# Kernel tuning notes

Hardware: AMD Instinct MI355X
Metric: run time of the kernel (lower is better)

## Reference

```python
import jax, jax.numpy as jnp
import numpy as np

EPS = 1e-5

def setup_inputs() -> dict:
    key = jax.random.key(0)
    k1, k2, k3, k4, k5 = jax.random.split(key, 5)
    x = jax.random.normal(k1, (2048, 64, 768), dtype=jnp.float32)
    ln_w = jnp.ones((768,), dtype=jnp.float32)
    ln_b = jnp.zeros((768,), dtype=jnp.float32)
    # nn.Linear default init: U(-1/sqrt(in), 1/sqrt(in))
    bound = 1.0 / np.sqrt(768.0)
    W = jax.random.uniform(k2, (64, 768), dtype=jnp.float32, minval=-bound, maxval=bound)
    b = jax.random.uniform(k3, (64,), dtype=jnp.float32, minval=-bound, maxval=bound)
    return {"x": x, "ln_w": ln_w, "ln_b": ln_b, "W": W, "b": b}

def reference(x, ln_w, ln_b, W, b):
    B = x.shape[0]
    # LayerNorm over last dim (768)
    mu = jnp.mean(x, axis=-1, keepdims=True)
    var = jnp.mean(jnp.square(x - mu), axis=-1, keepdims=True)
    xn = (x - mu) * jax.lax.rsqrt(var + EPS) * ln_w + ln_b
    # Linear 768 -> 64, then SiLU
    y = jnp.einsum('bch,oh->bco', xn, W) + b
    y = y * jax.nn.sigmoid(y)
    # unpatchify: [B,64,64] -> [B,8,8,4,4,4] -> permute(0,3,1,4,2,5) -> [B,4,32,32]
    y = y.reshape(B, 8, 8, 4, 4, 4)
    y = jnp.transpose(y, (0, 3, 1, 4, 2, 5))
    return y.reshape(B, 4, 32, 32)
```

## Files before the change

kernel.cpp:

```cpp
#include <hip/hip_runtime.h>
#include <hip/hip_bf16.h>
#include <cstdint>

typedef __attribute__((ext_vector_type(8))) short s16x8;
typedef __attribute__((ext_vector_type(4))) float f32x4;

union CV2 { __hip_bfloat162 h; uint32_t u; };

__global__ void prep_kernel(const float* __restrict__ W,
                            const float* __restrict__ lnw,
                            const float* __restrict__ lnb,
                            const float* __restrict__ bias,
                            __hip_bfloat16* __restrict__ Wb,
                            float* __restrict__ Ssum,
                            float* __restrict__ bp) {
    const int o = blockIdx.x;
    const int tid = threadIdx.x;
    float s = 0.f, bb = 0.f;
    for (int k = tid; k < 768; k += 256) {
        float wraw = W[o * 768 + k];
        float wv = lnw[k] * wraw;
        s += wv;
        bb += lnb[k] * wraw;
        int kk = k >> 5, rem = k & 31;
        int q = rem >> 3, j = rem & 7;
        int t = o >> 4, n = o & 15;
        int l = q * 16 + n;
        Wb[(kk * 4 + t) * 512 + l * 8 + j] = __float2bfloat16(wv);
    }
    __shared__ float rs[4], rb[4];
    for (int off = 32; off > 0; off >>= 1) {
        s  += __shfl_down(s, off);
        bb += __shfl_down(bb, off);
    }
    int wid = tid >> 6;
    if ((tid & 63) == 0) { rs[wid] = s; rb[wid] = bb; }
    __syncthreads();
    if (tid == 0) {
        Ssum[o] = rs[0] + rs[1] + rs[2] + rs[3];
        bp[o]   = bias[o] + rb[0] + rb[1] + rb[2] + rb[3];
    }
}

__global__ __launch_bounds__(256, 3) void fused_kernel(
        const float* __restrict__ x,
        const uint4* __restrict__ Wb4,
        const float* __restrict__ Ssum,
        const float* __restrict__ bp,
        float* __restrict__ out) {
    const int b   = blockIdx.x;
    const int tid = threadIdx.x;
    const int w   = tid >> 6;
    const int l   = tid & 63;
    const int q   = l >> 4;
    const int n   = l & 15;

    __shared__ __align__(16) float sout[4096];

    const float* xr = x + (size_t)b * 49152 + (w * 16 + n) * 768 + q * 8;
    const uint4* Wl = Wb4 + l;

    f32x4 acc0 = {0.f, 0.f, 0.f, 0.f};
    f32x4 acc1 = acc0, acc2 = acc0, acc3 = acc0;
    float sum = 0.f, ssq = 0.f;

    float4 cur[8], nxt[8];
    #pragma unroll
    for (int s = 0; s < 4; s++) {
        cur[2 * s]     = *(const float4*)(xr + s * 32);
        cur[2 * s + 1] = *(const float4*)(xr + s * 32 + 4);
    }

    #pragma unroll
    for (int c = 0; c < 6; c++) {
        s16x8 af[4];
        #pragma unroll
        for (int s = 0; s < 4; s++) {
            float4 lo = cur[2 * s], hi = cur[2 * s + 1];
            sum += lo.x; ssq = fmaf(lo.x, lo.x, ssq);
            sum += lo.y; ssq = fmaf(lo.y, lo.y, ssq);
            sum += lo.z; ssq = fmaf(lo.z, lo.z, ssq);
            sum += lo.w; ssq = fmaf(lo.w, lo.w, ssq);
            sum += hi.x; ssq = fmaf(hi.x, hi.x, ssq);
            sum += hi.y; ssq = fmaf(hi.y, hi.y, ssq);
            sum += hi.z; ssq = fmaf(hi.z, hi.z, ssq);
            sum += hi.w; ssq = fmaf(hi.w, hi.w, ssq);
            CV2 p0, p1, p2, p3;
            p0.h = __float22bfloat162_rn(make_float2(lo.x, lo.y));
            p1.h = __float22bfloat162_rn(make_float2(lo.z, lo.w));
            p2.h = __float22bfloat162_rn(make_float2(hi.x, hi.y));
            p3.h = __float22bfloat162_rn(make_float2(hi.z, hi.w));
            af[s] = __builtin_bit_cast(s16x8,
                        make_uint4(p0.u, p1.u, p2.u, p3.u));
        }

        if (c < 5) {
            #pragma unroll
            for (int s = 0; s < 4; s++) {
                nxt[2 * s]     = *(const float4*)(xr + (c + 1) * 128 + s * 32);
                nxt[2 * s + 1] = *(const float4*)(xr + (c + 1) * 128 + s * 32 + 4);
            }
        }

        #pragma unroll
        for (int s = 0; s < 4; s++) {
            uint4 wb0 = Wl[((c * 4 + s) * 4 + 0) * 64];
            uint4 wb1 = Wl[((c * 4 + s) * 4 + 1) * 64];
            uint4 wb2 = Wl[((c * 4 + s) * 4 + 2) * 64];
            uint4 wb3 = Wl[((c * 4 + s) * 4 + 3) * 64];
            acc0 = __builtin_amdgcn_mfma_f32_16x16x32_bf16(
                       af[s], __builtin_bit_cast(s16x8, wb0), acc0, 0, 0, 0);
            acc1 = __builtin_amdgcn_mfma_f32_16x16x32_bf16(
                       af[s], __builtin_bit_cast(s16x8, wb1), acc1, 0, 0, 0);
            acc2 = __builtin_amdgcn_mfma_f32_16x16x32_bf16(
                       af[s], __builtin_bit_cast(s16x8, wb2), acc2, 0, 0, 0);
            acc3 = __builtin_amdgcn_mfma_f32_16x16x32_bf16(
                       af[s], __builtin_bit_cast(s16x8, wb3), acc3, 0, 0, 0);
        }

        if (c < 5) {
            #pragma unroll
            for (int i = 0; i < 8; i++) cur[i] = nxt[i];
        }
    }

    sum += __shfl_xor(sum, 16); sum += __shfl_xor(sum, 32);
    ssq += __shfl_xor(ssq, 16); ssq += __shfl_xor(ssq, 32);
    const float mu   = sum * (1.0f / 768.0f);
    const float rstd = rsqrtf(ssq * (1.0f / 768.0f) - mu * mu + 1e-5f);

    float St[4], Bt[4];
    #pragma unroll
    for (int t = 0; t < 4; t++) {
        St[t] = Ssum[t * 16 + n];
        Bt[t] = bp[t * 16 + n];
    }

    const int o2 = (n >> 2) & 3;
    const int o3 = n & 3;
    f32x4 va[4] = {acc0, acc1, acc2, acc3};
    #pragma unroll
    for (int r = 0; r < 4; r++) {
        float mu_r   = __shfl(mu,   q * 4 + r);
        float rstd_r = __shfl(rstd, q * 4 + r);
        int cc  = w * 16 + q * 4 + r;
        int c1i = cc >> 3, c2i = cc & 7;
        int base = (c1i * 4 + o2) * 32 + c2i * 4 + o3;
        #pragma unroll
        for (int t = 0; t < 4; t++) {
            float y = rstd_r * (va[t][r] - mu_r * St[t]) + Bt[t];
            y = y / (1.0f + __expf(-y));
            sout[t * 1024 + base] = y;
        }
    }
    __syncthreads();

    float* outp = out + (size_t)b * 4096;
    #pragma unroll
    for (int j = 0; j < 4; j++) {
        *(float4*)(outp + j * 1024 + tid * 4) =
            *(const float4*)(&sout[j * 1024 + tid * 4]);
    }
}

extern "C" void kernel_launch(void* const* d_in, const int* in_sizes, int n_in,
                              void* d_out, int out_size, void* d_ws, size_t ws_size,
                              hipStream_t stream) {
    const float* x    = (const float*)d_in[0];
    const float* lnw  = (const float*)d_in[1];
    const float* lnb  = (const float*)d_in[2];
    const float* W    = (const float*)d_in[3];
    const float* bias = (const float*)d_in[4];
    float* out = (float*)d_out;

    const int B = in_sizes[0] / (64 * 768);

    __hip_bfloat16* Wb = (__hip_bfloat16*)d_ws;
    float* Ssum = (float*)((char*)d_ws + 98304);
    float* bp   = (float*)((char*)d_ws + 98304 + 256);

    prep_kernel<<<64, 256, 0, stream>>>(W, lnw, lnb, bias, Wb, Ssum, bp);
    fused_kernel<<<B, 256, 0, stream>>>(x, (const uint4*)d_ws, Ssum, bp, out);
}
```

Before: 613.7 us.

## Stage bf16 weights in LDS once per persistent block processing two batches

The fused kernel becomes a persistent grid-stride kernel of 512-thread blocks, with up to 256 blocks. Each block copies the whole 96 KB bf16 weight tile into LDS once and handles two batch elements per iteration. MFMA B-operands are then read from LDS instead of being re-fetched from global/L2 by every wave. The change also issues the next-chunk x prefetch before the current chunk's conversion. In exchange, 128 KB of LDS per block limits each CU to one block of 8 waves, which may reduce latency hiding for the streaming x loads.

Result: faster. 539.8 us (-12.0%).

```diff
diff --git a/kernel.cpp b/kernel.cpp
--- a/kernel.cpp
+++ b/kernel.cpp
@@ -42,92 +42,31 @@
     }
 }
 
-__global__ __launch_bounds__(256, 3) void fused_kernel(
+__global__ __launch_bounds__(512, 2) void fused_kernel(
         const float* __restrict__ x,
         const uint4* __restrict__ Wb4,
         const float* __restrict__ Ssum,
         const float* __restrict__ bp,
-        float* __restrict__ out) {
-    const int b   = blockIdx.x;
+        float* __restrict__ out,
+        int nb2) {
     const int tid = threadIdx.x;
     const int w   = tid >> 6;
     const int l   = tid & 63;
     const int q   = l >> 4;
     const int n   = l & 15;
-
-    __shared__ __align__(16) float sout[4096];
-
-    const float* xr = x + (size_t)b * 49152 + (w * 16 + n) * 768 + q * 8;
-    const uint4* Wl = Wb4 + l;
-
-    f32x4 acc0 = {0.f, 0.f, 0.f, 0.f};
-    f32x4 acc1 = acc0, acc2 = acc0, acc3 = acc0;
-    float sum = 0.f, ssq = 0.f;
-
-    float4 cur[8], nxt[8];
-    #pragma unroll
-    for (int s = 0; s < 4; s++) {
-        cur[2 * s]     = *(const float4*)(xr + s * 32);
-        cur[2 * s + 1] = *(const float4*)(xr + s * 32 + 4);
-    }
-
-    #pragma unroll
-    for (int c = 0; c < 6; c++) {
-        s16x8 af[4];
-        #pragma unroll
-        for (int s = 0; s < 4; s++) {
-            float4 lo = cur[2 * s], hi = cur[2 * s + 1];
-            sum += lo.x; ssq = fmaf(lo.x, lo.x, ssq);
-            sum += lo.y; ssq = fmaf(lo.y, lo.y, ssq);
-            sum += lo.z; ssq = fmaf(lo.z, lo.z, ssq);
-            sum += lo.w; ssq = fmaf(lo.w, lo.w, ssq);
-            sum += hi.x; ssq = fmaf(hi.x, hi.x, ssq);
-            sum += hi.y; ssq = fmaf(hi.y, hi.y, ssq);
-            sum += hi.z; ssq = fmaf(hi.z, hi.z, ssq);
-            sum += hi.w; ssq = fmaf(hi.w, hi.w, ssq);
-            CV2 p0, p1, p2, p3;
-            p0.h = __float22bfloat162_rn(make_float2(lo.x, lo.y));
-            p1.h = __float22bfloat162_rn(make_float2(lo.z, lo.w));
-            p2.h = __float22bfloat162_rn(make_float2(hi.x, hi.y));
-            p3.h = __float22bfloat162_rn(make_float2(hi.z, hi.w));
-            af[s] = __builtin_bit_cast(s16x8,
-                        make_uint4(p0.u, p1.u, p2.u, p3.u));
-        }
-
-        if (c < 5) {
-            #pragma unroll
-            for (int s = 0; s < 4; s++) {
-                nxt[2 * s]     = *(const float4*)(xr + (c + 1) * 128 + s * 32);
-                nxt[2 * s + 1] = *(const float4*)(xr + (c + 1) * 128 + s * 32 + 4);
-            }
-        }
-
-        #pragma unroll
-        for (int s = 0; s < 4; s++) {
-            uint4 wb0 = Wl[((c * 4 + s) * 4 + 0) * 64];
-            uint4 wb1 = Wl[((c * 4 + s) * 4 + 1) * 64];
-            uint4 wb2 = Wl[((c * 4 + s) * 4 + 2) * 64];
-            uint4 wb3 = Wl[((c * 4 + s) * 4 + 3) * 64];
-            acc0 = __builtin_amdgcn_mfma_f32_16x16x32_bf16(
-                       af[s], __builtin_bit_cast(s16x8, wb0), acc0, 0, 0, 0);
-            acc1 = __builtin_amdgcn_mfma_f32_16x16x32_bf16(
-                       af[s], __builtin_bit_cast(s16x8, wb1), acc1, 0, 0, 0);
-            acc2 = __builtin_amdgcn_mfma_f32_16x16x32_bf16(
-                       af[s], __builtin_bit_cast(s16x8, wb2), acc2, 0, 0, 0);
-            acc3 = __builtin_amdgcn_mfma_f32_16x16x32_bf16(
-                       af[s], __builtin_bit_cast(s16x8, wb3), acc3, 0, 0, 0);
-        }
-
-        if (c < 5) {
-            #pragma unroll
-            for (int i = 0; i < 8; i++) cur[i] = nxt[i];
-        }
-    }
-
-    sum += __shfl_xor(sum, 16); sum += __shfl_xor(sum, 32);
-    ssq += __shfl_xor(ssq, 16); ssq += __shfl_xor(ssq, 32);
-    const float mu   = sum * (1.0f / 768.0f);
-    const float rstd = rsqrtf(ssq * (1.0f / 768.0f) - mu * mu + 1e-5f);
+    const int wl  = w & 3;
+    const int bl  = w >> 2;
+
+    __shared__ __align__(16) char lds[98304 + 32768];
+
+    {
+        uint4* wlds = (uint4*)lds;
+        #pragma unroll
+        for (int j = 0; j < 12; j++) {
+            int idx = tid + j * 512;
+            wlds[idx] = Wb4[idx];
+        }
+    }
 
     float St[4], Bt[4];
     #pragma unroll
@@ -135,31 +74,111 @@
         St[t] = Ssum[t * 16 + n];
         Bt[t] = bp[t * 16 + n];
     }
+    __syncthreads();
 
     const int o2 = (n >> 2) & 3;
     const int o3 = n & 3;
-    f32x4 va[4] = {acc0, acc1, acc2, acc3};
-    #pragma unroll
-    for (int r = 0; r < 4; r++) {
-        float mu_r   = __shfl(mu,   q * 4 + r);
-        float rstd_r = __shfl(rstd, q * 4 + r);
-        int cc  = w * 16 + q * 4 + r;
-        int c1i = cc >> 3, c2i = cc & 7;
-        int base = (c1i * 4 + o2) * 32 + c2i * 4 + o3;
-        #pragma unroll
-        for (int t = 0; t < 4; t++) {
-            float y = rstd_r * (va[t][r] - mu_r * St[t]) + Bt[t];
-            y = y / (1.0f + __expf(-y));
-            sout[t * 1024 + base] = y;
-        }
-    }
-    __syncthreads();
-
-    float* outp = out + (size_t)b * 4096;
-    #pragma unroll
-    for (int j = 0; j < 4; j++) {
-        *(float4*)(outp + j * 1024 + tid * 4) =
-            *(const float4*)(&sout[j * 1024 + tid * 4]);
+    float* sout = (float*)(lds + 98304) + bl * 4096;
+
+    for (int b2 = blockIdx.x; b2 < nb2; b2 += gridDim.x) {
+        const float* xr = x + (size_t)(b2 * 2 + bl) * 49152
+                            + (wl * 16 + n) * 768 + q * 8;
+
+        f32x4 acc0 = {0.f, 0.f, 0.f, 0.f};
+        f32x4 acc1 = acc0, acc2 = acc0, acc3 = acc0;
+        float sum = 0.f, ssq = 0.f;
+
+        float4 cur[8], nxt[8];
+        #pragma unroll
+        for (int s = 0; s < 4; s++) {
+            cur[2 * s]     = *(const float4*)(xr + s * 32);
+            cur[2 * s + 1] = *(const float4*)(xr + s * 32 + 4);
+        }
+
+        #pragma unroll
+        for (int c = 0; c < 6; c++) {
+            if (c < 5) {
+                #pragma unroll
+                for (int s = 0; s < 4; s++) {
+                    nxt[2 * s]     = *(const float4*)(xr + (c + 1) * 128 + s * 32);
+                    nxt[2 * s + 1] = *(const float4*)(xr + (c + 1) * 128 + s * 32 + 4);
+                }
+            }
+
+            s16x8 af[4];
+            #pragma unroll
+            for (int s = 0; s < 4; s++) {
+                float4 lo = cur[2 * s], hi = cur[2 * s + 1];
+                sum += lo.x; ssq = fmaf(lo.x, lo.x, ssq);
+                sum += lo.y; ssq = fmaf(lo.y, lo.y, ssq);
+                sum += lo.z; ssq = fmaf(lo.z, lo.z, ssq);
+                sum += lo.w; ssq = fmaf(lo.w, lo.w, ssq);
+                sum += hi.x; ssq = fmaf(hi.x, hi.x, ssq);
+                sum += hi.y; ssq = fmaf(hi.y, hi.y, ssq);
+                sum += hi.z; ssq = fmaf(hi.z, hi.z, ssq);
+                sum += hi.w; ssq = fmaf(hi.w, hi.w, ssq);
+                CV2 p0, p1, p2, p3;
+                p0.h = __float22bfloat162_rn(make_float2(lo.x, lo.y));
+                p1.h = __float22bfloat162_rn(make_float2(lo.z, lo.w));
+                p2.h = __float22bfloat162_rn(make_float2(hi.x, hi.y));
+                p3.h = __float22bfloat162_rn(make_float2(hi.z, hi.w));
+                af[s] = __builtin_bit_cast(s16x8,
+                            make_uint4(p0.u, p1.u, p2.u, p3.u));
+            }
+
+            const char* wbp = lds + c * 16384 + l * 16;
+            #pragma unroll
+            for (int s = 0; s < 4; s++) {
+                uint4 wb0 = *(const uint4*)(wbp + (s * 4 + 0) * 1024);
+                uint4 wb1 = *(const uint4*)(wbp + (s * 4 + 1) * 1024);
+                uint4 wb2 = *(const uint4*)(wbp + (s * 4 + 2) * 1024);
+                uint4 wb3 = *(const uint4*)(wbp + (s * 4 + 3) * 1024);
+                acc0 = __builtin_amdgcn_mfma_f32_16x16x32_bf16(
+                           af[s], __builtin_bit_cast(s16x8, wb0), acc0, 0, 0, 0);
+                acc1 = __builtin_amdgcn_mfma_f32_16x16x32_bf16(
+                           af[s], __builtin_bit_cast(s16x8, wb1), acc1, 0, 0, 0);
+                acc2 = __builtin_amdgcn_mfma_f32_16x16x32_bf16(
+                           af[s], __builtin_bit_cast(s16x8, wb2), acc2, 0, 0, 0);
+                acc3 = __builtin_amdgcn_mfma_f32_16x16x32_bf16(
+                           af[s], __builtin_bit_cast(s16x8, wb3), acc3, 0, 0, 0);
+            }
+
+            if (c < 5) {
+                #pragma unroll
+                for (int i = 0; i < 8; i++) cur[i] = nxt[i];
+            }
+        }
+
+        sum += __shfl_xor(sum, 16); sum += __shfl_xor(sum, 32);
+        ssq += __shfl_xor(ssq, 16); ssq += __shfl_xor(ssq, 32);
+        const float mu   = sum * (1.0f / 768.0f);
+        const float rstd = rsqrtf(ssq * (1.0f / 768.0f) - mu * mu + 1e-5f);
+
+        f32x4 va[4] = {acc0, acc1, acc2, acc3};
+        #pragma unroll
+        for (int r = 0; r < 4; r++) {
+            float mu_r   = __shfl(mu,   q * 4 + r);
+            float rstd_r = __shfl(rstd, q * 4 + r);
+            int cc  = wl * 16 + q * 4 + r;
+            int c1i = cc >> 3, c2i = cc & 7;
+            int base = (c1i * 4 + o2) * 32 + c2i * 4 + o3;
+            #pragma unroll
+            for (int t = 0; t < 4; t++) {
+                float y = rstd_r * (va[t][r] - mu_r * St[t]) + Bt[t];
+                y = y / (1.0f + __expf(-y));
+                sout[t * 1024 + base] = y;
+            }
+        }
+        __syncthreads();
+
+        float* outp = out + (size_t)b2 * 8192;
+        const float* sfl = (const float*)(lds + 98304);
+        #pragma unroll
+        for (int j = 0; j < 4; j++) {
+            *(float4*)(outp + (j * 512 + tid) * 4) =
+                *(const float4*)(sfl + (j * 512 + tid) * 4);
+        }
+        __syncthreads();
     }
 }
 
@@ -180,5 +199,9 @@
     float* bp   = (float*)((char*)d_ws + 98304 + 256);
 
     prep_kernel<<<64, 256, 0, stream>>>(W, lnw, lnb, bias, Wb, Ssum, bp);
-    fused_kernel<<<B, 256, 0, stream>>>(x, (const uint4*)d_ws, Ssum, bp, out);
+
+    const int nb2  = B / 2;
+    const int grid = nb2 < 256 ? nb2 : 256;
+    fused_kernel<<<grid, 512, 0, stream>>>(x, (const uint4*)d_ws,
+                                           Ssum, bp, out, nb2);
 }
```
